# Kernel optimization log

Measured on AMD Instinct MI355X. Metric: run time of the kernel, lower is better.

## Reference

```python
import jax, jax.numpy as jnp
import numpy as np

DIM = 384
NUM_HEADS = 12
HEAD_DIM = 32
MID = NUM_HEADS * HEAD_DIM
RES = (32, 32)


def _relative_position_index(res):
    Hh, Ww = res
    coords = np.stack(np.meshgrid(np.arange(Hh), np.arange(Ww), indexing='ij'))  # 2,H,W
    cf = coords.reshape(2, -1)
    rel = cf[:, :, None] - cf[:, None, :]  # 2,N,N
    rel = rel.transpose(1, 2, 0).astype(np.int64)
    rel[:, :, 0] += Hh - 1
    rel[:, :, 1] += Ww - 1
    rel[:, :, 0] *= 2 * Ww - 1
    return rel.sum(-1)  # N,N


def setup_inputs() -> dict:
    key = jax.random.key(0)
    ks = jax.random.split(key, 8)
    B = 8
    Hh, Ww = RES
    table_size = (2 * Hh - 1) * (2 * Ww - 1)
    x = jax.random.normal(ks[0], (B, DIM, Hh, Ww), dtype=jnp.float32)
    wq = jax.random.normal(ks[1], (MID, DIM), dtype=jnp.float32) * 0.02
    bq = jnp.zeros((MID,), dtype=jnp.float32)
    wkv = jax.random.normal(ks[2], (2 * MID, DIM), dtype=jnp.float32) * 0.02
    bkv = jnp.zeros((2 * MID,), dtype=jnp.float32)
    wproj = jax.random.normal(ks[3], (DIM, MID), dtype=jnp.float32) * 0.02
    bproj = jnp.zeros((DIM,), dtype=jnp.float32)
    bias_table = jax.random.normal(ks[4], (table_size, NUM_HEADS), dtype=jnp.float32) * 0.02
    rel_index = jnp.asarray(_relative_position_index(RES), dtype=jnp.int32)  # N,N
    return {"x": x, "wq": wq, "bq": bq, "wkv": wkv, "bkv": bkv,
            "wproj": wproj, "bproj": bproj, "bias_table": bias_table,
            "rel_index": rel_index}


def reference(x, wq, bq, wkv, bkv, wproj, bproj, bias_table, rel_index):
    B, C, Hh, Ww = x.shape
    N = Hh * Ww
    scale = HEAD_DIM ** -0.5
    xf = x.reshape(B, C, N)  # B,C,N
    # 1x1 convs == channelwise linear
    q = jnp.einsum('oc,bcn->bon', wq, xf) + bq[None, :, None]          # B,MID,N
    kv = jnp.einsum('oc,bcn->bon', wkv, xf) + bkv[None, :, None]       # B,2*MID,N
    q = q.reshape(B, NUM_HEADS, HEAD_DIM, N).transpose(0, 1, 3, 2)     # B,h,N,d
    kv = kv.reshape(B, 2, NUM_HEADS, HEAD_DIM, N)
    k = kv[:, 0].transpose(0, 1, 3, 2)                                  # B,h,N,d
    v = kv[:, 1].transpose(0, 1, 3, 2)                                  # B,h,N,d
    attn = jnp.einsum('bhnd,bhmd->bhnm', q, k) * scale                  # B,h,N,N
    rel_bias = bias_table[rel_index.reshape(-1)].reshape(N, N, NUM_HEADS)
    attn = attn + rel_bias.transpose(2, 0, 1)[None]                     # + h,N,N bias
    attn = jax.nn.softmax(attn, axis=-1)
    out = jnp.einsum('bhnm,bhmd->bhnd', attn, v)                        # B,h,N,d
    out = out.transpose(0, 1, 3, 2).reshape(B, MID, N)                  # B,MID,N
    out = jnp.einsum('om,bmn->bon', wproj, out) + bproj[None, :, None]  # B,DIM,N
    return out.reshape(B, C, Hh, Ww)
```

## Files before the change

### kernel.cpp

```cpp
#include <hip/hip_runtime.h>

typedef __bf16 bf16;
typedef __bf16 bf16x8 __attribute__((ext_vector_type(8)));
typedef __bf16 bf16x4 __attribute__((ext_vector_type(4)));
typedef float  f32x4  __attribute__((ext_vector_type(4)));

static constexpr int NB = 8;
static constexpr int NH = 12;
static constexpr int HD = 32;
static constexpr int NN = 1024;
static constexpr int NC = 384;

static constexpr float LOG2E = 1.4426950408889634f;
static constexpr float QSC   = (float)(0.17677669529663687 * 1.4426950408889634);

static constexpr size_t XT_N   = (size_t)NB*NN*NC;
static constexpr size_t WQKV_N = (size_t)3*NC*NC;
static constexpr size_t WP_N   = (size_t)NC*NC;
static constexpr size_t QKV_N  = (size_t)NB*NH*NN*HD;
static constexpr size_t AO_N   = (size_t)NB*NN*NC;

static constexpr size_t XT_OFF   = 0;
static constexpr size_t WQKV_OFF = XT_OFF + XT_N;
static constexpr size_t WP_OFF   = WQKV_OFF + WQKV_N;
static constexpr size_t Q_OFF    = WP_OFF + WP_N;
static constexpr size_t K_OFF    = Q_OFF + QKV_N;
static constexpr size_t V_OFF    = K_OFF + QKV_N;
static constexpr size_t AO_OFF   = V_OFF + QKV_N;
static constexpr size_t PT_OFF   = AO_OFF + AO_N;

static constexpr int PT_PER_H = 63 * 62;
static constexpr int PT_TOTAL = NH * PT_PER_H;

#define MFMA16(a,b,c) __builtin_amdgcn_mfma_f32_16x16x32_bf16(a,b,c,0,0,0)

static __device__ inline float fast_exp2(float x) {
#if __has_builtin(__builtin_amdgcn_exp2f)
    return __builtin_amdgcn_exp2f(x);
#else
    return exp2f(x);
#endif
}

__global__ __launch_bounds__(256) void cast_all_kernel(const float* __restrict__ x,
                                                       const float* __restrict__ wq,
                                                       const float* __restrict__ wkv,
                                                       const float* __restrict__ wproj,
                                                       const float* __restrict__ bias_table,
                                                       bf16* __restrict__ xt,
                                                       bf16* __restrict__ wqkv,
                                                       bf16* __restrict__ wp,
                                                       unsigned* __restrict__ PT)
{
    __shared__ bf16 T[64][68];
    const int t = threadIdx.x;
    if (blockIdx.x >= 1344) {
        const int e = (blockIdx.x - 1344) * 256 + t;
        if (e >= PT_TOTAL) return;
        const int h = e / PT_PER_H, rem = e - h * PT_PER_H;
        const int dj = rem / 62, dip = rem - dj * 62;
        bf16 lo = (bf16)(bias_table[(size_t)((dip + 1) * 63 + dj) * NH + h] * LOG2E);
        bf16 hi = (bf16)(bias_table[(size_t)(dip * 63 + dj) * NH + h] * LOG2E);
        PT[e] = (unsigned)__builtin_bit_cast(unsigned short, lo)
              | ((unsigned)__builtin_bit_cast(unsigned short, hi) << 16);
        return;
    }
    if (blockIdx.x >= 768) {
        const size_t i = ((size_t)(blockIdx.x - 768) * 256 + t) * 4;
        if (i >= WQKV_N + WP_N) return;
        const float* src; bf16* dst;
        if (i < (size_t)NC*NC)      { src = wq + i;                     dst = wqkv + i; }
        else if (i < WQKV_N)        { src = wkv + (i - (size_t)NC*NC);  dst = wqkv + i; }
        else                        { src = wproj + (i - WQKV_N);       dst = wp + (i - WQKV_N); }
        float4 v = *(const float4*)src;
        bf16x4 o; o[0] = (bf16)v.x; o[1] = (bf16)v.y; o[2] = (bf16)v.z; o[3] = (bf16)v.w;
        *(bf16x4*)dst = o;
        return;
    }
    const int bid = blockIdx.x;
    const int b = bid / 96, rem = bid % 96, ct = rem >> 4, nt = rem & 15;
    const int c0 = ct * 64, n0 = nt * 64;
    const float* Xb = x + (size_t)b * NC * NN;
    const int nl = t & 63, c4 = (t >> 6) * 4;
#pragma unroll
    for (int i = 0; i < 4; ++i) {
        const int c = c4 + i * 16;
        bf16x4 v;
#pragma unroll
        for (int j = 0; j < 4; ++j)
            v[j] = (bf16)Xb[(size_t)(c0 + c + j) * NN + n0 + nl];
        *(bf16x4*)&T[nl][c] = v;
    }
    __syncthreads();
    const int n = t >> 2;
#pragma unroll
    for (int i = 0; i < 2; ++i) {
        const int cg = (t & 3) * 8 + i * 32;
        bf16x4 a = *(const bf16x4*)&T[n][cg];
        bf16x4 bv = *(const bf16x4*)&T[n][cg + 4];
        bf16x8 vv = __builtin_shufflevector(a, bv, 0, 1, 2, 3, 4, 5, 6, 7);
        *(bf16x8*)&xt[((size_t)b * NN + n0 + n) * NC + c0 + cg] = vv;
    }
}

__global__ __launch_bounds__(256) void qkv_gemm_kernel(
    const bf16* __restrict__ W, const bf16* __restrict__ Xt,
    const float* __restrict__ bq, const float* __restrict__ bkv,
    bf16* __restrict__ Qd, bf16* __restrict__ Kd, bf16* __restrict__ Vd)
{
    __shared__ bf16 As[128][72];
    __shared__ bf16 Bs[128][72];
    const int t = threadIdx.x;
    const int w = t >> 6, lane = t & 63, g = lane >> 4, l16 = lane & 15;
    const int wm = w >> 1, wn = w & 1;
    const int n0g = blockIdx.x * 128;
    const int b = n0g >> 10, n0 = n0g & 1023;
    const int o0 = blockIdx.y * 128;
    const bf16* Xb = Xt + (size_t)b * NN * NC;

    const int sr = t >> 1, sc2 = (t & 1) * 32;

    f32x4 acc[4][4] = {};

    bf16x8 aw[4], bw[4];
#pragma unroll
    for (int i = 0; i < 4; ++i) {
        aw[i] = *(const bf16x8*)&W [(size_t)(o0 + sr) * NC + sc2 + 8*i];
        bw[i] = *(const bf16x8*)&Xb[(size_t)(n0 + sr) * NC + sc2 + 8*i];
    }

    for (int k0 = 0; k0 < NC; k0 += 64) {
        __syncthreads();
#pragma unroll
        for (int i = 0; i < 4; ++i) {
            *(bf16x8*)&As[sr][sc2 + 8*i] = aw[i];
            *(bf16x8*)&Bs[sr][sc2 + 8*i] = bw[i];
        }
        __syncthreads();
        if (k0 + 64 < NC) {
#pragma unroll
            for (int i = 0; i < 4; ++i) {
                aw[i] = *(const bf16x8*)&W [(size_t)(o0 + sr) * NC + k0 + 64 + sc2 + 8*i];
                bw[i] = *(const bf16x8*)&Xb[(size_t)(n0 + sr) * NC + k0 + 64 + sc2 + 8*i];
            }
        }
#pragma unroll
        for (int ks = 0; ks < 2; ++ks) {
            bf16x8 a[4], bb[4];
#pragma unroll
            for (int s = 0; s < 4; ++s) {
                a[s]  = *(const bf16x8*)&As[wm*64 + s*16 + l16][ks*32 + g*8];
                bb[s] = *(const bf16x8*)&Bs[wn*64 + s*16 + l16][ks*32 + g*8];
            }
#pragma unroll
            for (int sm = 0; sm < 4; ++sm)
#pragma unroll
                for (int sn = 0; sn < 4; ++sn)
                    acc[sm][sn] = MFMA16(a[sm], bb[sn], acc[sm][sn]);
        }
    }

#pragma unroll
    for (int sm = 0; sm < 4; ++sm)
#pragma unroll
    for (int sn = 0; sn < 4; ++sn) {
        const int col   = n0 + wn*64 + sn*16 + l16;
        const int obase = o0 + wm*64 + sm*16 + g*4;
        f32x4 v = acc[sm][sn];
        if (obase < 384) {
            const int hh = obase >> 5, d = obase & 31;
            bf16x4 o4;
#pragma unroll
            for (int r = 0; r < 4; ++r) o4[r] = (bf16)((v[r] + bq[obase + r]) * QSC);
            *(bf16x4*)&Qd[(((size_t)b*NH + hh)*NN + col)*HD + d] = o4;
        } else if (obase < 768) {
            const int oo = obase - 384; const int hh = oo >> 5, d = oo & 31;
            bf16x4 o4;
#pragma unroll
            for (int r = 0; r < 4; ++r) o4[r] = (bf16)(v[r] + bkv[oo + r]);
            *(bf16x4*)&Kd[(((size_t)b*NH + hh)*NN + col)*HD + d] = o4;
        } else {
            const int oo = obase - 768; const int hh = oo >> 5, d = oo & 31;
#pragma unroll
            for (int r = 0; r < 4; ++r)
                Vd[(((size_t)b*NH + hh)*HD + d + r)*NN + col] = (bf16)(v[r] + bkv[obase - 384 + r]);
        }
    }
}

__global__ __launch_bounds__(512, 4) void attn_kernel(
    const bf16* __restrict__ Qg, const bf16* __restrict__ Kg, const bf16* __restrict__ Vg,
    const unsigned* __restrict__ PT, bf16* __restrict__ AOt)
{
    __shared__ __align__(16) char arena[28032];
    bf16 (*KsH)[64][40]    = (bf16 (*)[64][40])arena;
    bf16 (*VsH)[32][72]    = (bf16 (*)[32][72])(arena + 10240);
    unsigned (*pairTw)[34] = (unsigned (*)[34])(arena + 19456);

    const int t = threadIdx.x;
    const int w = t >> 6, lane = t & 63, g = lane >> 4, l16 = lane & 15;
    const int wl = w & 3, hf = w >> 2;

    const int bid = blockIdx.x;
    const int nid = (bid & 7) * 96 + (bid >> 3);
    const int qt = nid & 7;
    const int hb = nid >> 3;
    const int h = hb % 12, b = hb / 12;

    const bf16* Qb = Qg + ((size_t)(b*NH + h)) * NN * HD;
    const bf16* Kb = Kg + ((size_t)(b*NH + h)) * NN * HD;
    const bf16* Vb = Vg + ((size_t)(b*NH + h)) * HD * NN;

    const int tl = t & 255, g2 = t >> 8;
    const int kr = tl >> 2, kc2 = (tl & 3) * 8;
    const int vd = tl >> 3, vmb = (tl & 7) * 8;
    const int vqa = ((vmb >> 5) & 1) * 32 + ((vmb >> 2) & 3) * 8 + ((vmb >> 4) & 1) * 4;
    const int mbase = g2 * 512;

    bf16x8 sregK = *(const bf16x8*)&Kb[(size_t)(mbase + kr) * HD + kc2];
    bf16x8 sregV = *(const bf16x8*)&Vb[(size_t)vd * NN + mbase + vmb];

    const int q0 = qt * 128;
    const bf16x8 qfrag0 = *(const bf16x8*)&Qb[(size_t)(q0 + wl*32      + l16) * HD + g*8];
    const bf16x8 qfrag1 = *(const bf16x8*)&Qb[(size_t)(q0 + wl*32 + 16 + l16) * HD + g*8];

    const unsigned* PTh = PT + (size_t)h * PT_PER_H + 4 * qt;
    for (int idx = t; idx < 63 * 34; idx += 512) {
        const int dj = idx / 34, dipl = idx - dj * 34;
        pairTw[dj][dipl] = PTh[dj * 62 + dipl];
    }

    const unsigned* twp = &pairTw[0][0];
    const int rowD1 = (l16 + 31 - 4*g) * 34;

    bf16x8 vones;
#pragma unroll
    for (int e = 0; e < 8; ++e) vones[e] = (bf16)1.0f;

    f32x4 oacc0[2] = {}, oacc1[2] = {};
    f32x4 oacc_l0 = {}, oacc_l1 = {};

    for (int ph = 0; ph < 8; ++ph) {
        __syncthreads();
        *(bf16x8*)&KsH[g2][kr][kc2] = sregK;
        { bf16x4 vlo = __builtin_shufflevector(sregV, sregV, 0, 1, 2, 3);
          bf16x4 vhi = __builtin_shufflevector(sregV, sregV, 4, 5, 6, 7);
          *(bf16x4*)&VsH[g2][vd][vqa]     = vlo;
          *(bf16x4*)&VsH[g2][vd][vqa + 8] = vhi; }
        __syncthreads();
        if (ph < 7) {
            const int m1 = mbase + (ph + 1) * 64;
            sregK = *(const bf16x8*)&Kb[(size_t)(m1 + kr) * HD + kc2];
            sregV = *(const bf16x8*)&Vb[(size_t)vd * NN + m1 + vmb];
        }

        {
            const int it = hf * 8 + ph;
            const bf16 (*Vsp)[72] = VsH[hf];
            const int dipl = wl + 30 - 2*it;
            const unsigned* pD1 = twp + rowD1 + dipl;

            f32x4 b00, b01, b02, b03, b10, b12;
#pragma unroll
            for (int r = 0; r < 4; ++r) {
                const unsigned d1w = pD1[-34 * r];
                const unsigned d0w = pD1[-34 * r - 544];
                const unsigned d2w = pD1[-34 * r + 544];
                b00[r] = __uint_as_float(d1w << 16);
                b02[r] = __uint_as_float(d1w & 0xFFFF0000u);
                b01[r] = __uint_as_float(d0w << 16);
                b03[r] = __uint_as_float(d0w & 0xFFFF0000u);
                b10[r] = __uint_as_float(d2w << 16);
                b12[r] = __uint_as_float(d2w & 0xFFFF0000u);
            }
            f32x4 bacc0[4] = {b00, b01, b02, b03};
            f32x4 bacc1[4] = {b10, b00, b12, b02};

            bf16x8 pa0[2], pa1[2];
#pragma unroll
            for (int sc = 0; sc < 4; ++sc) {
                bf16x8 kf = *(const bf16x8*)&KsH[hf][sc*16 + l16][g*8];
                f32x4 z0 = MFMA16(kf, qfrag0, bacc0[sc]);
                f32x4 z1 = MFMA16(kf, qfrag1, bacc1[sc]);
                const int kc = sc >> 1, hl = (sc & 1) * 4;
#pragma unroll
                for (int r = 0; r < 4; ++r) {
                    pa0[kc][hl + r] = (bf16)fast_exp2(z0[r]);
                    pa1[kc][hl + r] = (bf16)fast_exp2(z1[r]);
                }
            }

#pragma unroll
            for (int kc = 0; kc < 2; ++kc) {
#pragma unroll
                for (int ds = 0; ds < 2; ++ds) {
                    bf16x8 vf = *(const bf16x8*)&Vsp[ds*16 + l16][kc*32 + 8*g];
                    oacc0[ds] = MFMA16(pa0[kc], vf, oacc0[ds]);
                    oacc1[ds] = MFMA16(pa1[kc], vf, oacc1[ds]);
                }
                oacc_l0 = MFMA16(pa0[kc], vones, oacc_l0);
                oacc_l1 = MFMA16(pa1[kc], vones, oacc_l1);
            }
        }
    }

    __syncthreads();
    f32x4* mbuf = (f32x4*)arena;
    const int sb = wl * 64 + lane;
    if (hf == 1) {
        mbuf[0*256 + sb] = oacc0[0]; mbuf[1*256 + sb] = oacc0[1];
        mbuf[2*256 + sb] = oacc1[0]; mbuf[3*256 + sb] = oacc1[1];
        mbuf[4*256 + sb] = oacc_l0;  mbuf[5*256 + sb] = oacc_l1;
    }
    __syncthreads();
    if (hf == 0) {
        oacc0[0] += mbuf[0*256 + sb]; oacc0[1] += mbuf[1*256 + sb];
        oacc1[0] += mbuf[2*256 + sb]; oacc1[1] += mbuf[3*256 + sb];
        oacc_l0  += mbuf[4*256 + sb]; oacc_l1  += mbuf[5*256 + sb];

        float rin0[4], rin1[4];
#pragma unroll
        for (int r = 0; r < 4; ++r) {
            rin0[r] = 1.0f / oacc_l0[r];
            rin1[r] = 1.0f / oacc_l1[r];
        }
        const int nrow0 = q0 + wl*32 + g*4;
#pragma unroll
        for (int ds = 0; ds < 2; ++ds) {
            const int c = h*HD + ds*16 + l16;
#pragma unroll
            for (int r = 0; r < 4; ++r) {
                AOt[((size_t)b*NN + nrow0 + r)      * NC + c] = (bf16)(oacc0[ds][r] * rin0[r]);
                AOt[((size_t)b*NN + nrow0 + 16 + r) * NC + c] = (bf16)(oacc1[ds][r] * rin1[r]);
            }
        }
    }
}

__global__ __launch_bounds__(256) void proj_gemm_kernel(
    const bf16* __restrict__ W, const bf16* __restrict__ AOt,
    const float* __restrict__ bproj, float* __restrict__ out)
{
    __shared__ bf16 As[64][40];
    __shared__ bf16 Bs[64][40];
    const int t = threadIdx.x;
    const int w = t >> 6, lane = t & 63, g = lane >> 4, l16 = lane & 15;
    const int wm = w >> 1, wn = w & 1;
    const int n0g = blockIdx.x * 64;
    const int b = n0g >> 10, n0 = n0g & 1023;
    const int o0 = blockIdx.y * 64;
    const bf16* Ab = AOt + (size_t)b * NN * NC;

    const int sr = t >> 2, sc = (t & 3) * 8;

    f32x4 acc[2][2] = {};

    bf16x8 aw = *(const bf16x8*)&W [(size_t)(o0 + sr) * NC + sc];
    bf16x8 bw = *(const bf16x8*)&Ab[(size_t)(n0 + sr) * NC + sc];

    for (int k0 = 0; k0 < NC; k0 += 32) {
        __syncthreads();
        *(bf16x8*)&As[sr][sc] = aw;
        *(bf16x8*)&Bs[sr][sc] = bw;
        __syncthreads();
        if (k0 + 32 < NC) {
            aw = *(const bf16x8*)&W [(size_t)(o0 + sr) * NC + k0 + 32 + sc];
            bw = *(const bf16x8*)&Ab[(size_t)(n0 + sr) * NC + k0 + 32 + sc];
        }
        bf16x8 a[2], bb[2];
#pragma unroll
        for (int s = 0; s < 2; ++s) {
            a[s]  = *(const bf16x8*)&As[wm*32 + s*16 + l16][g*8];
            bb[s] = *(const bf16x8*)&Bs[wn*32 + s*16 + l16][g*8];
        }
#pragma unroll
        for (int sm = 0; sm < 2; ++sm)
#pragma unroll
            for (int sn = 0; sn < 2; ++sn)
                acc[sm][sn] = MFMA16(a[sm], bb[sn], acc[sm][sn]);
    }

#pragma unroll
    for (int sm = 0; sm < 2; ++sm)
#pragma unroll
    for (int sn = 0; sn < 2; ++sn) {
        const int col   = n0 + wn*32 + sn*16 + l16;
        const int obase = o0 + wm*32 + sm*16 + g*4;
        f32x4 v = acc[sm][sn];
#pragma unroll
        for (int r = 0; r < 4; ++r)
            out[((size_t)b*NC + obase + r)*NN + col] = v[r] + bproj[obase + r];
    }
}

extern "C" void kernel_launch(void* const* d_in, const int* in_sizes, int n_in,
                              void* d_out, int out_size, void* d_ws, size_t ws_size,
                              hipStream_t stream)
{
    const float* x          = (const float*)d_in[0];
    const float* wq         = (const float*)d_in[1];
    const float* bq         = (const float*)d_in[2];
    const float* wkv        = (const float*)d_in[3];
    const float* bkv        = (const float*)d_in[4];
    const float* wproj      = (const float*)d_in[5];
    const float* bproj      = (const float*)d_in[6];
    const float* bias_table = (const float*)d_in[7];
    float* out = (float*)d_out;

    bf16* wsb  = (bf16*)d_ws;
    bf16* Xt   = wsb + XT_OFF;
    bf16* Wqkv = wsb + WQKV_OFF;
    bf16* Wp   = wsb + WP_OFF;
    bf16* Qd   = wsb + Q_OFF;
    bf16* Kd   = wsb + K_OFF;
    bf16* Vd   = wsb + V_OFF;
    bf16* AOt  = wsb + AO_OFF;
    unsigned* PT = (unsigned*)(wsb + PT_OFF);

    const int ptBlocks = (PT_TOTAL + 255) / 256;
    cast_all_kernel<<<dim3(768 + 576 + ptBlocks), 256, 0, stream>>>(
        x, wq, wkv, wproj, bias_table, Xt, Wqkv, Wp, PT);
    qkv_gemm_kernel<<<dim3(64, 9), 256, 0, stream>>>(Wqkv, Xt, bq, bkv, Qd, Kd, Vd);
    attn_kernel<<<dim3(768), 512, 0, stream>>>(Qd, Kd, Vd, PT, AOt);
    proj_gemm_kernel<<<dim3(128, 6), 256, 0, stream>>>(Wp, AOt, bproj, out);
}
```

Before: 65.21 us.

## Load K/V fragments directly from global into registers, drop LDS staging and split-K

The attention kernel no longer stages K and V tiles through shared memory. Each wave now loads its MFMA fragments straight from global memory into double-buffered registers. The QKV GEMM writes V with a permuted column order so the direct loads match the fragment layout. The two-half split over keys and its LDS reduction are removed, and the block shrinks to 256 threads that each walk all 16 key tiles. This removes LDS traffic and barriers, but every wave re-reads K/V from global or L2, register pressure rises, and parallelism per block halves.

```diff
diff --git a/kernel.cpp b/kernel.cpp
--- a/kernel.cpp
+++ b/kernel.cpp
@@ -181,25 +181,22 @@
             *(bf16x4*)&Kd[(((size_t)b*NH + hh)*NN + col)*HD + d] = o4;
         } else {
             const int oo = obase - 768; const int hh = oo >> 5, d = oo & 31;
+            const int pcol = (col & ~0x1C) | (((col >> 2) & 3) << 3) | (((col >> 4) & 1) << 2);
 #pragma unroll
             for (int r = 0; r < 4; ++r)
-                Vd[(((size_t)b*NH + hh)*HD + d + r)*NN + col] = (bf16)(v[r] + bkv[obase - 384 + r]);
-        }
-    }
-}
-
-__global__ __launch_bounds__(512, 4) void attn_kernel(
+                Vd[(((size_t)b*NH + hh)*HD + d + r)*NN + pcol] = (bf16)(v[r] + bkv[obase - 384 + r]);
+        }
+    }
+}
+
+__global__ __launch_bounds__(256, 3) void attn_kernel(
     const bf16* __restrict__ Qg, const bf16* __restrict__ Kg, const bf16* __restrict__ Vg,
     const unsigned* __restrict__ PT, bf16* __restrict__ AOt)
 {
-    __shared__ __align__(16) char arena[28032];
-    bf16 (*KsH)[64][40]    = (bf16 (*)[64][40])arena;
-    bf16 (*VsH)[32][72]    = (bf16 (*)[32][72])(arena + 10240);
-    unsigned (*pairTw)[34] = (unsigned (*)[34])(arena + 19456);
+    __shared__ unsigned int pairTw[63][34];
 
     const int t = threadIdx.x;
     const int w = t >> 6, lane = t & 63, g = lane >> 4, l16 = lane & 15;
-    const int wl = w & 3, hf = w >> 2;
 
     const int bid = blockIdx.x;
     const int nid = (bid & 7) * 96 + (bid >> 3);
@@ -211,24 +208,27 @@
     const bf16* Kb = Kg + ((size_t)(b*NH + h)) * NN * HD;
     const bf16* Vb = Vg + ((size_t)(b*NH + h)) * HD * NN;
 
-    const int tl = t & 255, g2 = t >> 8;
-    const int kr = tl >> 2, kc2 = (tl & 3) * 8;
-    const int vd = tl >> 3, vmb = (tl & 7) * 8;
-    const int vqa = ((vmb >> 5) & 1) * 32 + ((vmb >> 2) & 3) * 8 + ((vmb >> 4) & 1) * 4;
-    const int mbase = g2 * 512;
-
-    bf16x8 sregK = *(const bf16x8*)&Kb[(size_t)(mbase + kr) * HD + kc2];
-    bf16x8 sregV = *(const bf16x8*)&Vb[(size_t)vd * NN + mbase + vmb];
-
     const int q0 = qt * 128;
-    const bf16x8 qfrag0 = *(const bf16x8*)&Qb[(size_t)(q0 + wl*32      + l16) * HD + g*8];
-    const bf16x8 qfrag1 = *(const bf16x8*)&Qb[(size_t)(q0 + wl*32 + 16 + l16) * HD + g*8];
+
+    const bf16x8 qfrag0 = *(const bf16x8*)&Qb[(size_t)(q0 + w*32      + l16) * HD + g*8];
+    const bf16x8 qfrag1 = *(const bf16x8*)&Qb[(size_t)(q0 + w*32 + 16 + l16) * HD + g*8];
+
+    bf16x8 kf[2][4], vf[2][4];
+#pragma unroll
+    for (int sc = 0; sc < 4; ++sc)
+        kf[0][sc] = *(const bf16x8*)&Kb[(size_t)(sc*16 + l16) * HD + g*8];
+#pragma unroll
+    for (int kc = 0; kc < 2; ++kc)
+#pragma unroll
+        for (int ds = 0; ds < 2; ++ds)
+            vf[0][kc*2 + ds] = *(const bf16x8*)&Vb[(size_t)(ds*16 + l16) * NN + kc*32 + 8*g];
 
     const unsigned* PTh = PT + (size_t)h * PT_PER_H + 4 * qt;
-    for (int idx = t; idx < 63 * 34; idx += 512) {
+    for (int idx = t; idx < 63 * 34; idx += 256) {
         const int dj = idx / 34, dipl = idx - dj * 34;
         pairTw[dj][dipl] = PTh[dj * 62 + dipl];
     }
+    __syncthreads();
 
     const unsigned* twp = &pairTw[0][0];
     const int rowD1 = (l16 + 31 - 4*g) * 34;
@@ -240,99 +240,80 @@
     f32x4 oacc0[2] = {}, oacc1[2] = {};
     f32x4 oacc_l0 = {}, oacc_l1 = {};
 
-    for (int ph = 0; ph < 8; ++ph) {
-        __syncthreads();
-        *(bf16x8*)&KsH[g2][kr][kc2] = sregK;
-        { bf16x4 vlo = __builtin_shufflevector(sregV, sregV, 0, 1, 2, 3);
-          bf16x4 vhi = __builtin_shufflevector(sregV, sregV, 4, 5, 6, 7);
-          *(bf16x4*)&VsH[g2][vd][vqa]     = vlo;
-          *(bf16x4*)&VsH[g2][vd][vqa + 8] = vhi; }
-        __syncthreads();
-        if (ph < 7) {
-            const int m1 = mbase + (ph + 1) * 64;
-            sregK = *(const bf16x8*)&Kb[(size_t)(m1 + kr) * HD + kc2];
-            sregV = *(const bf16x8*)&Vb[(size_t)vd * NN + m1 + vmb];
-        }
-
-        {
-            const int it = hf * 8 + ph;
-            const bf16 (*Vsp)[72] = VsH[hf];
-            const int dipl = wl + 30 - 2*it;
-            const unsigned* pD1 = twp + rowD1 + dipl;
-
-            f32x4 b00, b01, b02, b03, b10, b12;
+#pragma unroll
+    for (int it = 0; it < 16; ++it) {
+        const int cur = it & 1, nxt = cur ^ 1;
+        if (it < 15) {
+            const int m1 = (it + 1) * 64;
+#pragma unroll
+            for (int sc = 0; sc < 4; ++sc)
+                kf[nxt][sc] = *(const bf16x8*)&Kb[(size_t)(m1 + sc*16 + l16) * HD + g*8];
+#pragma unroll
+            for (int kc = 0; kc < 2; ++kc)
+#pragma unroll
+                for (int ds = 0; ds < 2; ++ds)
+                    vf[nxt][kc*2 + ds] = *(const bf16x8*)&Vb[(size_t)(ds*16 + l16) * NN + m1 + kc*32 + 8*g];
+        }
+
+        const int dipl = w + 30 - 2*it;
+        const unsigned* pD1 = twp + rowD1 + dipl;
+
+        f32x4 b00, b01, b02, b03, b10, b12;
+#pragma unroll
+        for (int r = 0; r < 4; ++r) {
+            const unsigned d1w = pD1[-34 * r];
+            const unsigned d0w = pD1[-34 * r - 544];
+            const unsigned d2w = pD1[-34 * r + 544];
+            b00[r] = __uint_as_float(d1w << 16);
+            b02[r] = __uint_as_float(d1w & 0xFFFF0000u);
+            b01[r] = __uint_as_float(d0w << 16);
+            b03[r] = __uint_as_float(d0w & 0xFFFF0000u);
+            b10[r] = __uint_as_float(d2w << 16);
+            b12[r] = __uint_as_float(d2w & 0xFFFF0000u);
+        }
+        f32x4 bacc0[4] = {b00, b01, b02, b03};
+        f32x4 bacc1[4] = {b10, b00, b12, b02};
+
+        bf16x8 pa0[2], pa1[2];
+#pragma unroll
+        for (int sc = 0; sc < 4; ++sc) {
+            f32x4 z0 = MFMA16(kf[cur][sc], qfrag0, bacc0[sc]);
+            f32x4 z1 = MFMA16(kf[cur][sc], qfrag1, bacc1[sc]);
+            const int kc = sc >> 1, hl = (sc & 1) * 4;
 #pragma unroll
             for (int r = 0; r < 4; ++r) {
-                const unsigned d1w = pD1[-34 * r];
-                const unsigned d0w = pD1[-34 * r - 544];
-                const unsigned d2w = pD1[-34 * r + 544];
-                b00[r] = __uint_as_float(d1w << 16);
-                b02[r] = __uint_as_float(d1w & 0xFFFF0000u);
-                b01[r] = __uint_as_float(d0w << 16);
-                b03[r] = __uint_as_float(d0w & 0xFFFF0000u);
-                b10[r] = __uint_as_float(d2w << 16);
-                b12[r] = __uint_as_float(d2w & 0xFFFF0000u);
+                pa0[kc][hl + r] = (bf16)fast_exp2(z0[r]);
+                pa1[kc][hl + r] = (bf16)fast_exp2(z1[r]);
             }
-            f32x4 bacc0[4] = {b00, b01, b02, b03};
-            f32x4 bacc1[4] = {b10, b00, b12, b02};
-
-            bf16x8 pa0[2], pa1[2];
-#pragma unroll
-            for (int sc = 0; sc < 4; ++sc) {
-                bf16x8 kf = *(const bf16x8*)&KsH[hf][sc*16 + l16][g*8];
-                f32x4 z0 = MFMA16(kf, qfrag0, bacc0[sc]);
-                f32x4 z1 = MFMA16(kf, qfrag1, bacc1[sc]);
-                const int kc = sc >> 1, hl = (sc & 1) * 4;
-#pragma unroll
-                for (int r = 0; r < 4; ++r) {
-                    pa0[kc][hl + r] = (bf16)fast_exp2(z0[r]);
-                    pa1[kc][hl + r] = (bf16)fast_exp2(z1[r]);
-                }
+        }
+
+#pragma unroll
+        for (int kc = 0; kc < 2; ++kc) {
+#pragma unroll
+            for (int ds = 0; ds < 2; ++ds) {
+                oacc0[ds] = MFMA16(pa0[kc], vf[cur][kc*2 + ds], oacc0[ds]);
+                oacc1[ds] = MFMA16(pa1[kc], vf[cur][kc*2 + ds], oacc1[ds]);
             }
-
-#pragma unroll
-            for (int kc = 0; kc < 2; ++kc) {
-#pragma unroll
-                for (int ds = 0; ds < 2; ++ds) {
-                    bf16x8 vf = *(const bf16x8*)&Vsp[ds*16 + l16][kc*32 + 8*g];
-                    oacc0[ds] = MFMA16(pa0[kc], vf, oacc0[ds]);
-                    oacc1[ds] = MFMA16(pa1[kc], vf, oacc1[ds]);
-                }
-                oacc_l0 = MFMA16(pa0[kc], vones, oacc_l0);
-                oacc_l1 = MFMA16(pa1[kc], vones, oacc_l1);
-            }
-        }
-    }
-
-    __syncthreads();
-    f32x4* mbuf = (f32x4*)arena;
-    const int sb = wl * 64 + lane;
-    if (hf == 1) {
-        mbuf[0*256 + sb] = oacc0[0]; mbuf[1*256 + sb] = oacc0[1];
-        mbuf[2*256 + sb] = oacc1[0]; mbuf[3*256 + sb] = oacc1[1];
-        mbuf[4*256 + sb] = oacc_l0;  mbuf[5*256 + sb] = oacc_l1;
-    }
-    __syncthreads();
-    if (hf == 0) {
-        oacc0[0] += mbuf[0*256 + sb]; oacc0[1] += mbuf[1*256 + sb];
-        oacc1[0] += mbuf[2*256 + sb]; oacc1[1] += mbuf[3*256 + sb];
-        oacc_l0  += mbuf[4*256 + sb]; oacc_l1  += mbuf[5*256 + sb];
-
-        float rin0[4], rin1[4];
+            oacc_l0 = MFMA16(pa0[kc], vones, oacc_l0);
+            oacc_l1 = MFMA16(pa1[kc], vones, oacc_l1);
+        }
+    }
+
+    float rin0[4], rin1[4];
+#pragma unroll
+    for (int r = 0; r < 4; ++r) {
+        rin0[r] = 1.0f / oacc_l0[r];
+        rin1[r] = 1.0f / oacc_l1[r];
+    }
+
+    const int nrow0 = q0 + w*32 + g*4;
+#pragma unroll
+    for (int ds = 0; ds < 2; ++ds) {
+        const int c = h*HD + ds*16 + l16;
 #pragma unroll
         for (int r = 0; r < 4; ++r) {
-            rin0[r] = 1.0f / oacc_l0[r];
-            rin1[r] = 1.0f / oacc_l1[r];
-        }
-        const int nrow0 = q0 + wl*32 + g*4;
-#pragma unroll
-        for (int ds = 0; ds < 2; ++ds) {
-            const int c = h*HD + ds*16 + l16;
-#pragma unroll
-            for (int r = 0; r < 4; ++r) {
-                AOt[((size_t)b*NN + nrow0 + r)      * NC + c] = (bf16)(oacc0[ds][r] * rin0[r]);
-                AOt[((size_t)b*NN + nrow0 + 16 + r) * NC + c] = (bf16)(oacc1[ds][r] * rin1[r]);
-            }
+            AOt[((size_t)b*NN + nrow0 + r)      * NC + c] = (bf16)(oacc0[ds][r] * rin0[r]);
+            AOt[((size_t)b*NN + nrow0 + 16 + r) * NC + c] = (bf16)(oacc1[ds][r] * rin1[r]);
         }
     }
 }
@@ -421,6 +402,6 @@
     cast_all_kernel<<<dim3(768 + 576 + ptBlocks), 256, 0, stream>>>(
         x, wq, wkv, wproj, bias_table, Xt, Wqkv, Wp, PT);
     qkv_gemm_kernel<<<dim3(64, 9), 256, 0, stream>>>(Wqkv, Xt, bq, bkv, Qd, Kd, Vd);
-    attn_kernel<<<dim3(768), 512, 0, stream>>>(Qd, Kd, Vd, PT, AOt);
+    attn_kernel<<<dim3(768), 256, 0, stream>>>(Qd, Kd, Vd, PT, AOt);
     proj_gemm_kernel<<<dim3(128, 6), 256, 0, stream>>>(Wp, AOt, bproj, out);
 }
```

Result: slower. 76.05 us (+16.6%).
